# Kernel optimization log

Measured on AMD Instinct MI355X. Metric: run time of the kernel, lower is better.

Reference implementation:

```python
import jax, jax.numpy as jnp
import numpy as np

IN_CH, HID, OUT_CH = 1, 16, 1

def _conv(x, w, b, pad):
    # x: [B,C,H,W], w: [O,I,kh,kw], b: [O]
    y = jax.lax.conv_general_dilated(
        x, w, window_strides=(1, 1), padding=[(pad, pad), (pad, pad)],
        dimension_numbers=('NCHW', 'OIHW', 'NCHW'))
    return y + b[None, :, None, None]

def setup_inputs() -> dict:
    key = jax.random.key(0)
    ks = jax.random.split(key, 8)
    def w_init(k, shape):
        fan_in = shape[1] * shape[2] * shape[3]
        return jax.random.normal(k, shape, dtype=jnp.float32) * (1.0 / np.sqrt(fan_in))
    B, H, W = 32, 256, 256
    return {
        'x': jax.random.normal(ks[0], (B, IN_CH, H, W), dtype=jnp.float32),
        'w_perceive': w_init(ks[1], (HID * 2, IN_CH + HID, 3, 3)),
        'b_perceive': jnp.zeros((HID * 2,), jnp.float32),
        'w_up1': w_init(ks[2], (HID, HID * 2, 1, 1)),
        'b_up1': jnp.zeros((HID,), jnp.float32),
        'w_up2': w_init(ks[3], (HID, HID, 1, 1)),
        'b_up2': jnp.zeros((HID,), jnp.float32),
        'w_tau': w_init(ks[4], (HID, IN_CH + HID * 2, 3, 3)),
        'b_tau_conv': jnp.zeros((HID,), jnp.float32),
        'b_tau': jnp.ones((1, HID, 1, 1), jnp.float32) * 1.5,
        'w_read': w_init(ks[5], (OUT_CH, HID, 1, 1)),
        'b_read': jnp.zeros((OUT_CH,), jnp.float32),
        'n_steps': 10,
    }

def reference(x, w_perceive, b_perceive, w_up1, b_up1, w_up2, b_up2,
              w_tau, b_tau_conv, b_tau, w_read, b_read, n_steps):
    B, _, H, W = x.shape
    state = jnp.zeros((B, HID, H, W), dtype=x.dtype)

    def step(state, _):
        combined = jnp.concatenate([x, state], axis=1)          # [B, in+hid, H, W]
        perception = _conv(combined, w_perceive, b_perceive, 1)  # [B, 2*hid, H, W]
        h1 = jax.nn.relu(_conv(perception, w_up1, b_up1, 0))
        delta = _conv(h1, w_up2, b_up2, 0)                       # [B, hid, H, W]
        tau_input = jnp.concatenate([x, state, delta], axis=1)  # [B, in+2*hid, H, W]
        tau_logit = _conv(tau_input, w_tau, b_tau_conv, 1) + b_tau
        beta = jnp.clip(jax.nn.sigmoid(tau_logit), 0.01, 0.99)
        return beta * state + (1.0 - beta) * delta, None

    state, _ = jax.lax.scan(step, state, None, length=n_steps)
    return jax.nn.sigmoid(_conv(state, w_read, b_read, 0))
```

## Files before the change

kernel.cpp:

```cpp
#include <hip/hip_runtime.h>
#include <hip/hip_bf16.h>
#include <math.h>


#define B_   32
#define H_   256
#define W_   256
#define PIT  40
#define HP   36
#define XPP  260

typedef unsigned short ushort_t;
typedef __attribute__((ext_vector_type(8))) short short8;
typedef __attribute__((ext_vector_type(4))) float float4v;

__device__ __forceinline__ unsigned fbits(float f) {
    union { float f; unsigned u; } v; v.f = f; return v.u;
}
__device__ __forceinline__ ushort_t f2bu(float f) {
    return (ushort_t)((fbits(f) + 0x8000u) >> 16);
}
__device__ __forceinline__ unsigned pack2(float lo, float hi) {
    return ((fbits(hi) + 0x8000u) & 0xFFFF0000u) | ((fbits(lo) + 0x8000u) >> 16);
}
__device__ __forceinline__ float bu2f(ushort_t u) {
    union { unsigned i; float f; } v; v.i = ((unsigned)u) << 16; return v.f;
}
__device__ __forceinline__ float lo2f(unsigned u) {
    union { unsigned i; float f; } v; v.i = u << 16; return v.f;
}
__device__ __forceinline__ float hi2f(unsigned u) {
    union { unsigned i; float f; } v; v.i = u & 0xFFFF0000u; return v.f;
}

__global__ void prep(
    const float* __restrict__ wp,
    const float* __restrict__ wu1,
    const float* __restrict__ bu1,
    const float* __restrict__ bp,
    const float* __restrict__ wu2,
    const float* __restrict__ wt,
    ushort_t* __restrict__ wh1p,
    ushort_t* __restrict__ wu2f,
    ushort_t* __restrict__ wtn,
    float* __restrict__ scal)
{
    __shared__ float Weff[16 * 153];
    const int tid = threadIdx.x;

    for (int i = tid; i < 16 * 153; i += 256) {
        int j = i / 153, rem = i % 153, c = rem / 9, t = rem % 9;
        float s = 0.f;
        for (int o = 0; o < 32; ++o)
            s += wu1[j * 32 + o] * wp[o * 153 + c * 9 + t];
        Weff[i] = s;
    }
    if (tid < 16) {
        float s = bu1[tid];
        for (int o = 0; o < 32; ++o) s += wu1[tid * 32 + o] * bp[o];
        scal[tid] = s;
    }
    __syncthreads();

    if (tid < 16) scal[16 + tid] = Weff[tid * 153 + 8];

    for (int i = tid; i < 4 * 64 * 8; i += 256) {
        int ii = i >> 9, lane = (i >> 3) & 63, j = i & 7;
        int n = lane & 15, kk = ((lane >> 4) << 3) + j;
        int tap = 2 * ii + (kk >> 4), ch = kk & 15;
        wh1p[i] = f2bu(Weff[n * 153 + (ch + 1) * 9 + tap]);
    }
    for (int i = tid; i < 512; i += 256) {
        int lane = i >> 3, j = i & 7;
        int n = lane & 15, k = ((lane >> 4) << 3) + j;
        float v = 0.f;
        if (k < 16)      v = Weff[n * 153 + (k + 1) * 9 + 8];
        else if (k < 24) v = Weff[n * 153 + (k - 16)];
        wh1p[2048 + i] = f2bu(v);
    }
    for (int i = tid; i < 512; i += 256) {
        int lane = i >> 3, j = i & 7;
        int n = lane & 15, k = ((lane >> 4) << 3) + j;
        wu2f[i] = (k < 16) ? f2bu(wu2[n * 16 + k]) : (ushort_t)0;
    }
    for (int i = tid; i < 9 * 64 * 8; i += 256) {
        int t = i / 512, lane = (i / 8) % 64, j = i % 8;
        int n = lane & 15, k = ((lane >> 4) << 3) + j;
        int c = (k < 16) ? (17 + k) : (k - 15);
        wtn[i] = f2bu(wt[n * 297 + c * 9 + t]);
    }
}

__global__ __launch_bounds__(256) void precompute_tx(
    const float* __restrict__ x,
    const float* __restrict__ wt,
    const float* __restrict__ btc,
    const float* __restrict__ bt,
    ushort_t* __restrict__ tx)
{
    int p = blockIdx.x * 256 + threadIdx.x;
    int py = (p >> 8) & 255, px = p & 255;
    const float* xb = x + (p & ~0xFFFF);

    float xp[9];
#pragma unroll
    for (int t = 0; t < 9; ++t) {
        int gy = py + t / 3 - 1, gx = px + t % 3 - 1;
        bool in = ((unsigned)gy < 256u) & ((unsigned)gx < 256u);
        xp[t] = in ? xb[gy * 256 + gx] : 0.f;
    }
    short8 o0, o1;
#pragma unroll
    for (int j = 0; j < 16; ++j) {
        float tv = btc[j] + bt[j];
#pragma unroll
        for (int t = 0; t < 9; ++t) tv = fmaf(xp[t], wt[j * 297 + t], tv);
        if (j < 8) o0[j] = (short)f2bu(tv); else o1[j - 8] = (short)f2bu(tv);
    }
    ushort_t* dst = tx + (size_t)p * 16;
    *(short8*)(dst)     = o0;
    *(short8*)(dst + 8) = o1;
}

__global__ __launch_bounds__(256) void precompute_xp8(
    const float* __restrict__ x,
    ushort_t* __restrict__ xp8)
{
    int idx = blockIdx.x * 256 + threadIdx.x;
    if (idx >= B_ * XPP * XPP) return;
    int b  = idx / (XPP * XPP), rem = idx - b * (XPP * XPP);
    int by = rem / XPP, bx = rem - by * XPP;
    int gy = by - 2, gx = bx - 2;
    const float* xb = x + (size_t)b * 65536;
    short8 v;
#pragma unroll
    for (int t = 0; t < 8; ++t) {
        int yy = gy + t / 3, xx = gx + t % 3;
        bool in = ((unsigned)yy < 256u) & ((unsigned)xx < 256u);
        v[t] = in ? (short)f2bu(xb[yy * 256 + xx]) : (short)0;
    }
    *(short8*)(xp8 + (size_t)idx * 8) = v;
}

__global__ __launch_bounds__(256) void nca_step(
    const ushort_t* __restrict__ stIn,
    ushort_t* __restrict__ stOut,
    const ushort_t* __restrict__ xp8g,
    const ushort_t* __restrict__ txg,
    const ushort_t* __restrict__ wh1p,
    const ushort_t* __restrict__ wu2f,
    const ushort_t* __restrict__ wtn,
    const float* __restrict__ scal,
    const float* __restrict__ bu2G,
    const float* __restrict__ wrd,
    const float* __restrict__ brd,
    float* __restrict__ outg,
    int first, int last)
{
    __shared__ ushort_t comb[400 * PIT];
    __shared__ ushort_t hgrp[64 * HP];
    __shared__ ushort_t dump[256];

    const int tid  = threadIdx.x;
    const int w    = tid >> 6, lane = tid & 63;
    const int m    = lane & 15, q = lane >> 4;
    const int och  = q * 4;
    const int gx0  = blockIdx.x * 16, gy0 = blockIdx.y * 16;
    const size_t pb = (size_t)blockIdx.z * 65536;
    const size_t xpb = (size_t)blockIdx.z * (XPP * XPP);
    const short8 z8 = {0, 0, 0, 0, 0, 0, 0, 0};
    const float4v z4 = {0.f, 0.f, 0.f, 0.f};

    short8 wh1r[5], wtnr[9];
#pragma unroll
    for (int i = 0; i < 5; ++i) wh1r[i] = *(const short8*)(wh1p + (i * 64 + lane) * 8);
#pragma unroll
    for (int t = 0; t < 9; ++t) wtnr[t] = *(const short8*)(wtn + (t * 64 + lane) * 8);
    const short8 wu2r = *(const short8*)(wu2f + lane * 8);

    float4v beff4, wxh84, bu24, wr4;
#pragma unroll
    for (int r = 0; r < 4; ++r) {
        beff4[r] = scal[och + r];
        wxh84[r] = scal[16 + och + r];
        bu24[r]  = bu2G[och + r];
        wr4[r]   = wrd[och + r];
    }
    const float br = brd[0];

    const int sel = q >> 1;
    int offp[4];
#pragma unroll
    for (int ii = 0; ii < 4; ++ii) {
        int tA = 2 * ii, tB = 2 * ii + 1;
        int oA = ((tA / 3) * 20 + (tA % 3)) * PIT;
        int oB = ((tB / 3) * 20 + (tB % 3)) * PIT;
        offp[ii] = sel ? oB : oA;
    }
    const int chOff = 16 + (q & 1) * 8;
    const int t8off = (2 * 20 + 2) * PIT;
    const int off5  = (q == 0) ? (t8off + 16) : (q == 1) ? (t8off + 24)
                    : (q == 2) ? 32 : 16;

    for (int p = tid; p < 400; p += 256) {
        int ry = p / 20, rx = p - ry * 20;
        int gy = gy0 + ry - 2, gx = gx0 + rx - 2;
        ushort_t* row = comb + p * PIT;
        bool in = ((unsigned)gy < 256u) & ((unsigned)gx < 256u);
        if (in && !first) {
            const ushort_t* sp = stIn + (pb + gy * 256 + gx) * 16;
            *(short8*)(row + 16) = *(const short8*)(sp);
            *(short8*)(row + 24) = *(const short8*)(sp + 8);
        } else {
            *(short8*)(row + 16) = z8; *(short8*)(row + 24) = z8;
        }
        *(short8*)(row + 32) = *(const short8*)(
            xp8g + (xpb + (size_t)(gy0 + ry) * XPP + (gx0 + rx)) * 8);
    }
    if (tid < 128)
        *(short8*)(hgrp + (tid >> 1) * HP + 16 + (tid & 1) * 8) = z8;
    __syncthreads();

    ushort_t* hg = hgrp + (w * 16 + m) * HP;
    for (int i = 0; i < 6; ++i) {
        int g = w + 4 * i; if (g >= 21) break;
        int raw = g * 16 + m;
        int idx = (raw > 323) ? 323 : raw;
        int py = idx / 18, px = idx - py * 18;
        const ushort_t* abase = comb + (py * 20 + px) * PIT;
        float4v acc = z4;
#pragma unroll
        for (int ii = 0; ii < 4; ++ii) {
            short8 b = *(const short8*)(abase + offp[ii] + chOff);
            acc = __builtin_amdgcn_mfma_f32_16x16x32_bf16(wh1r[ii], b, acc, 0, 0, 0);
        }
        {
            short8 b = *(const short8*)(abase + off5);
            acc = __builtin_amdgcn_mfma_f32_16x16x32_bf16(wh1r[4], b, acc, 0, 0, 0);
        }
        float x8 = bu2f(comb[((py + 2) * 20 + px + 2) * PIT + 32]);
        uint2 hv;
        {
            float h0 = fmaxf(acc[0] + beff4[0] + x8 * wxh84[0], 0.f);
            float h1 = fmaxf(acc[1] + beff4[1] + x8 * wxh84[1], 0.f);
            float h2 = fmaxf(acc[2] + beff4[2] + x8 * wxh84[2], 0.f);
            float h3 = fmaxf(acc[3] + beff4[3] + x8 * wxh84[3], 0.f);
            hv.x = pack2(h0, h1); hv.y = pack2(h2, h3);
        }
        *(uint2*)(hg + och) = hv;
        __threadfence_block();
        short8 b2 = *(const short8*)(hgrp + (w * 16 + m) * HP + q * 8);
        float4v d = __builtin_amdgcn_mfma_f32_16x16x32_bf16(wu2r, b2, z4, 0, 0, 0);
        bool vld = raw < 324;
        int gy = gy0 - 1 + py, gx = gx0 - 1 + px;
        bool im = vld & ((unsigned)gy < 256u) & ((unsigned)gx < 256u);
        uint2 dv;
        dv.x = pack2(d[0] + bu24[0], d[1] + bu24[1]);
        dv.y = pack2(d[2] + bu24[2], d[3] + bu24[3]);
        if (!im) { dv.x = 0u; dv.y = 0u; }
        uint2* dst = vld ? (uint2*)(comb + ((py + 1) * 20 + (px + 1)) * PIT + och)
                         : (uint2*)(dump + (lane << 2));
        *dst = dv;
        __threadfence_block();
    }
    __syncthreads();

    for (int i = 0; i < 4; ++i) {
        int g = w * 4 + i;
        const ushort_t* cb = comb + ((g + 1) * 20 + (m + 1)) * PIT;
        float4v acc = z4;
#pragma unroll
        for (int t = 0; t < 9; ++t) {
            short8 b = *(const short8*)(cb + ((t / 3) * 20 + (t % 3)) * PIT + q * 8);
            acc = __builtin_amdgcn_mfma_f32_16x16x32_bf16(wtnr[t], b, acc, 0, 0, 0);
        }
        int gy = gy0 + g;
        const size_t pix = pb + gy * 256 + gx0 + m;
        const ushort_t* cpx = comb + ((g + 2) * 20 + (m + 2)) * PIT;
        uint2 su = *(const uint2*)(cpx + 16 + och);
        uint2 du = *(const uint2*)(cpx + och);
        uint2 tu = *(const uint2*)(txg + pix * 16 + och);
        float sold[4] = { lo2f(su.x), hi2f(su.x), lo2f(su.y), hi2f(su.y) };
        float dvv[4]  = { lo2f(du.x), hi2f(du.x), lo2f(du.y), hi2f(du.y) };
        float txv[4]  = { lo2f(tu.x), hi2f(tu.x), lo2f(tu.y), hi2f(tu.y) };
        float sn[4];
#pragma unroll
        for (int r = 0; r < 4; ++r) {
            float tl  = acc[r] + txv[r];
            float e   = __expf(-tl);
            float bta = __builtin_amdgcn_rcpf(1.f + e);
            bta = fminf(fmaxf(bta, 0.01f), 0.99f);
            sn[r] = dvv[r] + bta * (sold[r] - dvv[r]);
        }
        if (!last) {
            uint2 o;
            o.x = pack2(sn[0], sn[1]); o.y = pack2(sn[2], sn[3]);
            *(uint2*)(stOut + pix * 16 + och) = o;
        } else {
            float v = sn[0] * wr4[0] + sn[1] * wr4[1]
                    + sn[2] * wr4[2] + sn[3] * wr4[3];
            v += __shfl_xor(v, 16);
            v += __shfl_xor(v, 32);
            if (q == 0) {
                float eo = __expf(-(v + br));
                outg[pix] = __builtin_amdgcn_rcpf(1.f + eo);
            }
        }
    }
}

extern "C" void kernel_launch(void* const* d_in, const int* in_sizes, int n_in,
                              void* d_out, int out_size, void* d_ws, size_t ws_size,
                              hipStream_t stream)
{
    const float* x          = (const float*)d_in[0];
    const float* w_perceive = (const float*)d_in[1];
    const float* b_perceive = (const float*)d_in[2];
    const float* w_up1      = (const float*)d_in[3];
    const float* b_up1      = (const float*)d_in[4];
    const float* w_up2      = (const float*)d_in[5];
    const float* b_up2      = (const float*)d_in[6];
    const float* w_tau      = (const float*)d_in[7];
    const float* b_tau_conv = (const float*)d_in[8];
    const float* b_tau      = (const float*)d_in[9];
    const float* w_read     = (const float*)d_in[10];
    const float* b_read     = (const float*)d_in[11];
    float* out = (float*)d_out;

    const size_t stateElems = (size_t)B_ * H_ * W_ * 16;
    const size_t xp8Elems   = (size_t)B_ * XPP * XPP * 8;

    ushort_t* stA  = (ushort_t*)d_ws;
    ushort_t* stB  = stA + stateElems;
    ushort_t* txg  = stB + stateElems;
    ushort_t* xp8g = txg + stateElems;
    ushort_t* wh1p = xp8g + xp8Elems;
    ushort_t* wu2f = wh1p + 2560;
    ushort_t* wtn  = wu2f + 512;
    float*    scal = (float*)(wtn + 4608);

    const size_t needBytes = (3 * stateElems + xp8Elems
                              + 2560 + 512 + 4608) * sizeof(ushort_t)
                           + 32 * sizeof(float);
    if (ws_size < needBytes) return;

    prep<<<dim3(1), dim3(256), 0, stream>>>(
        w_perceive, w_up1, b_up1, b_perceive, w_up2, w_tau,
        wh1p, wu2f, wtn, scal);
    precompute_tx<<<dim3(8192), dim3(256), 0, stream>>>(
        x, w_tau, b_tau_conv, b_tau, txg);
    precompute_xp8<<<dim3((B_ * XPP * XPP + 255) / 256), dim3(256), 0, stream>>>(
        x, xp8g);

    ushort_t* cur = stA;
    ushort_t* nxt = stB;
    for (int s = 0; s < 10; ++s) {
        nca_step<<<dim3(16, 16, 32), dim3(256), 0, stream>>>(
            cur, nxt, xp8g, txg, wh1p, wu2f, wtn, scal, b_up2,
            w_read, b_read, out, (s == 0) ? 1 : 0, (s == 9) ? 1 : 0);
        ushort_t* t = cur; cur = nxt; nxt = t;
    }
}
```

Before: 818.3 us.

## Reshuffle hidden activations via ds_bpermute and prefetch tau inputs early

```diff
diff --git a/kernel.cpp b/kernel.cpp
--- a/kernel.cpp
+++ b/kernel.cpp
@@ -7,7 +7,6 @@
 #define H_   256
 #define W_   256
 #define PIT  40
-#define HP   36
 #define XPP  260
 
 typedef unsigned short ushort_t;
@@ -158,8 +157,6 @@
     int first, int last)
 {
     __shared__ ushort_t comb[400 * PIT];
-    __shared__ ushort_t hgrp[64 * HP];
-    __shared__ ushort_t dump[256];
 
     const int tid  = threadIdx.x;
     const int w    = tid >> 6, lane = tid & 63;
@@ -171,6 +168,13 @@
     const short8 z8 = {0, 0, 0, 0, 0, 0, 0, 0};
     const float4v z4 = {0.f, 0.f, 0.f, 0.f};
 
+    uint2 tpre[4];
+#pragma unroll
+    for (int i = 0; i < 4; ++i) {
+        const size_t pix = pb + (size_t)(gy0 + w * 4 + i) * 256 + gx0 + m;
+        tpre[i] = *(const uint2*)(txg + pix * 16 + och);
+    }
+
     short8 wh1r[5], wtnr[9];
 #pragma unroll
     for (int i = 0; i < 5; ++i) wh1r[i] = *(const short8*)(wh1p + (i * 64 + lane) * 8);
@@ -201,6 +205,9 @@
     const int t8off = (2 * 20 + 2) * PIT;
     const int off5  = (q == 0) ? (t8off + 16) : (q == 1) ? (t8off + 24)
                     : (q == 2) ? 32 : 16;
+
+    const int bpA = ((m + (q << 5)) & 63) << 2;
+    const bool hiq = q >= 2;
 
     for (int p = tid; p < 400; p += 256) {
         int ry = p / 20, rx = p - ry * 20;
@@ -217,11 +224,8 @@
         *(short8*)(row + 32) = *(const short8*)(
             xp8g + (xpb + (size_t)(gy0 + ry) * XPP + (gx0 + rx)) * 8);
     }
-    if (tid < 128)
-        *(short8*)(hgrp + (tid >> 1) * HP + 16 + (tid & 1) * 8) = z8;
     __syncthreads();
 
-    ushort_t* hg = hgrp + (w * 16 + m) * HP;
     for (int i = 0; i < 6; ++i) {
         int g = w + 4 * i; if (g >= 21) break;
         int raw = g * 16 + m;
@@ -247,10 +251,14 @@
             float h3 = fmaxf(acc[3] + beff4[3] + x8 * wxh84[3], 0.f);
             hv.x = pack2(h0, h1); hv.y = pack2(h2, h3);
         }
-        *(uint2*)(hg + och) = hv;
-        __threadfence_block();
-        short8 b2 = *(const short8*)(hgrp + (w * 16 + m) * HP + q * 8);
-        float4v d = __builtin_amdgcn_mfma_f32_16x16x32_bf16(wu2r, b2, z4, 0, 0, 0);
+        int vx0 = __builtin_amdgcn_ds_bpermute(bpA,      (int)hv.x);
+        int vy0 = __builtin_amdgcn_ds_bpermute(bpA,      (int)hv.y);
+        int vx1 = __builtin_amdgcn_ds_bpermute(bpA + 64, (int)hv.x);
+        int vy1 = __builtin_amdgcn_ds_bpermute(bpA + 64, (int)hv.y);
+        union { int i4[4]; short8 s8; } bb;
+        bb.i4[0] = hiq ? 0 : vx0;  bb.i4[1] = hiq ? 0 : vy0;
+        bb.i4[2] = hiq ? 0 : vx1;  bb.i4[3] = hiq ? 0 : vy1;
+        float4v d = __builtin_amdgcn_mfma_f32_16x16x32_bf16(wu2r, bb.s8, z4, 0, 0, 0);
         bool vld = raw < 324;
         int gy = gy0 - 1 + py, gx = gx0 - 1 + px;
         bool im = vld & ((unsigned)gy < 256u) & ((unsigned)gx < 256u);
@@ -258,10 +266,8 @@
         dv.x = pack2(d[0] + bu24[0], d[1] + bu24[1]);
         dv.y = pack2(d[2] + bu24[2], d[3] + bu24[3]);
         if (!im) { dv.x = 0u; dv.y = 0u; }
-        uint2* dst = vld ? (uint2*)(comb + ((py + 1) * 20 + (px + 1)) * PIT + och)
-                         : (uint2*)(dump + (lane << 2));
-        *dst = dv;
-        __threadfence_block();
+        if (vld)
+            *(uint2*)(comb + ((py + 1) * 20 + (px + 1)) * PIT + och) = dv;
     }
     __syncthreads();
 
@@ -279,7 +285,7 @@
         const ushort_t* cpx = comb + ((g + 2) * 20 + (m + 2)) * PIT;
         uint2 su = *(const uint2*)(cpx + 16 + och);
         uint2 du = *(const uint2*)(cpx + och);
-        uint2 tu = *(const uint2*)(txg + pix * 16 + och);
+        uint2 tu = tpre[i];
         float sold[4] = { lo2f(su.x), hi2f(su.x), lo2f(su.y), hi2f(su.y) };
         float dvv[4]  = { lo2f(du.x), hi2f(du.x), lo2f(du.y), hi2f(du.y) };
         float txv[4]  = { lo2f(tu.x), hi2f(tu.x), lo2f(tu.y), hi2f(tu.y) };
```

After: 786.7 us. -3.9%, faster.
